# Kernel tuning notes

Hardware: AMD Instinct MI355X
Metric: run time of the kernel (lower is better)

The kernel has to match this reference:

```python
import jax, jax.numpy as jnp
import numpy as np

MULT = 32       # multiplicity per irrep type (both input and output)
N = 262144      # number of nodes/examples
LS = (0, 1, 2, 3)  # irrep degrees -> block sizes 2l+1 = 1,3,5,7


def setup_inputs() -> dict:
    key = jax.random.key(0)
    keys = jax.random.split(key, 2 * len(LS))
    inp = {}
    for j, l in enumerate(LS):
        m = 2 * l + 1
        inp[f"x{l}"] = jax.random.normal(keys[2 * j], (N, MULT, m), dtype=jnp.float32)
        inp[f"W{l}"] = jax.random.normal(keys[2 * j + 1], (MULT, MULT, m), dtype=jnp.float32)
    return inp


def reference(x0, x1, x2, x3, W0, W1, W2, W3):
    # Block-diagonal equivariant linear: for each irrep type l,
    # out[n, o, m] = sum_i W_l[o, i, m] * x_l[n, i, m]
    # (elementwise in m within each 2l+1 block, summed over input multiplicity i).
    outs = [
        jnp.einsum("nim,oim->nom", x, W)
        for x, W in ((x0, W0), (x1, W1), (x2, W2), (x3, W3))
    ]
    # Concatenate flattened irrep blocks -> [N, MULT*(1+3+5+7)] = [N, 512]
    return jnp.concatenate([o.reshape(o.shape[0], -1) for o in outs], axis=-1)
```

## Files before the change

### kernel.cpp

```cpp
#include <hip/hip_runtime.h>
#include <hip/hip_fp16.h>


#define NTH 512
#define TN  32

typedef _Float16 f16x8 __attribute__((ext_vector_type(8)));
typedef float    f32x4 __attribute__((ext_vector_type(4)));

template<int M_, int PB>
__device__ __forceinline__ void stage(const float* __restrict__ src,
                                      __half* __restrict__ dst, int tid)
{
    #pragma unroll
    for (int it = 0; it < (256 * M_ + NTH - 1) / NTH; ++it) {
        const int f = tid + it * NTH;
        if (f < 256 * M_) {
            float4 v = ((const float4*)src)[f];
            const int e0 = 4 * f;
            if (M_ == 1) {
                const int node = e0 >> 5, i = e0 & 31;
                __half2* p = (__half2*)(dst + node * 40 + i);
                p[0] = __floats2half2_rn(v.x, v.y);
                p[1] = __floats2half2_rn(v.z, v.w);
            } else {
                const float vf[4] = {v.x, v.y, v.z, v.w};
                #pragma unroll
                for (int k = 0; k < 4; ++k) {
                    const int e    = e0 + k;
                    const int node = e / (32 * M_);
                    const int r    = e - node * (32 * M_);
                    const int i    = r / M_, mi = r - i * M_;
                    dst[(PB + mi) * 1280 + node * 40 + i] = __float2half(vf[k]);
                }
            }
        }
    }
}

__device__ __forceinline__ void plane_info(int p, int& Mm, int& BASE, int& MI)
{
    if (p == 0)     { Mm = 1; BASE = 0;   MI = 0;     }
    else if (p < 4) { Mm = 3; BASE = 32;  MI = p - 1; }
    else if (p < 9) { Mm = 5; BASE = 128; MI = p - 4; }
    else            { Mm = 7; BASE = 288; MI = p - 9; }
}

__global__ __launch_bounds__(NTH, 4) void eqlin(
    const float* __restrict__ x0, const float* __restrict__ x1,
    const float* __restrict__ x2, const float* __restrict__ x3,
    const float* __restrict__ w0, const float* __restrict__ w1,
    const float* __restrict__ w2, const float* __restrict__ w3,
    float* __restrict__ out, int n_tiles)
{
    __shared__ __align__(16) __half XT[20480];
    __shared__ __align__(16) __half WT[20480];
    const int tid  = threadIdx.x;
    const int wave = tid >> 6;
    const int lane = tid & 63;

    stage<1, 0>(w0, WT, tid);
    stage<3, 1>(w1, WT, tid);
    stage<5, 4>(w2, WT, tid);
    stage<7, 9>(w3, WT, tid);

    int Mm0, BASE0, MI0, Mm1, BASE1, MI1;
    plane_info(wave * 2,     Mm0, BASE0, MI0);
    plane_info(wave * 2 + 1, Mm1, BASE1, MI1);

    const int lrow = lane & 15;
    const int lk8  = (lane >> 4) * 8;
    const int crow = (lane >> 4) * 4;

    for (int t = blockIdx.x; t < n_tiles; t += gridDim.x) {
        const long node0 = (long)t * TN;
        __syncthreads();
        stage<1, 0>(x0 + node0 * 32,  XT, tid);
        stage<3, 1>(x1 + node0 * 96,  XT, tid);
        stage<5, 4>(x2 + node0 * 160, XT, tid);
        stage<7, 9>(x3 + node0 * 224, XT, tid);
        __syncthreads();

        f32x4 acc[2][2][2] = {};
        #pragma unroll
        for (int pl = 0; pl < 2; ++pl) {
            const int plane = wave * 2 + pl;
            const __half* xb = XT + plane * 1280 + lrow * 40 + lk8;
            const __half* wb = WT + plane * 1280 + lrow * 40 + lk8;
            f16x8 A0 = *(const f16x8*)xb;
            f16x8 A1 = *(const f16x8*)(xb + 640);
            f16x8 B0 = *(const f16x8*)wb;
            f16x8 B1 = *(const f16x8*)(wb + 640);
            acc[pl][0][0] = __builtin_amdgcn_mfma_f32_16x16x32_f16(A0, B0, acc[pl][0][0], 0, 0, 0);
            acc[pl][0][1] = __builtin_amdgcn_mfma_f32_16x16x32_f16(A0, B1, acc[pl][0][1], 0, 0, 0);
            acc[pl][1][0] = __builtin_amdgcn_mfma_f32_16x16x32_f16(A1, B0, acc[pl][1][0], 0, 0, 0);
            acc[pl][1][1] = __builtin_amdgcn_mfma_f32_16x16x32_f16(A1, B1, acc[pl][1][1], 0, 0, 0);
        }
        __syncthreads();

        __half* OUT = XT;
        #pragma unroll
        for (int pl = 0; pl < 2; ++pl) {
            const int Mm   = pl ? Mm1   : Mm0;
            const int BASE = pl ? BASE1 : BASE0;
            const int MI   = pl ? MI1   : MI0;
            #pragma unroll
            for (int nh = 0; nh < 2; ++nh)
            #pragma unroll
            for (int oh = 0; oh < 2; ++oh) {
                const int o     = oh * 16 + lrow;
                const int colb  = BASE + o * Mm + MI;
                const int nodeb = nh * 16 + crow;
                #pragma unroll
                for (int r = 0; r < 4; ++r)
                    OUT[(nodeb + r) * 520 + colb] = __float2half(acc[pl][nh][oh][r]);
            }
        }
        __syncthreads();

        float* dst = out + node0 * 512;
        #pragma unroll
        for (int it = 0; it < 4; ++it) {
            const int d0   = 8 * tid + 4096 * it;
            const int node = d0 >> 9, col = d0 & 511;
            uint4 h8 = *(const uint4*)(OUT + node * 520 + col);
            const __half2* hp = (const __half2*)&h8;
            float2 f0 = __half22float2(hp[0]);
            float2 f1 = __half22float2(hp[1]);
            float2 f2 = __half22float2(hp[2]);
            float2 f3 = __half22float2(hp[3]);
            *(float4*)(dst + d0)     = make_float4(f0.x, f0.y, f1.x, f1.y);
            *(float4*)(dst + d0 + 4) = make_float4(f2.x, f2.y, f3.x, f3.y);
        }
    }
}

extern "C" void kernel_launch(void* const* d_in, const int* in_sizes, int n_in,
                              void* d_out, int out_size, void* d_ws, size_t ws_size,
                              hipStream_t stream)
{
    long tot = 0;
    for (int i = 0; i < n_in; ++i) tot += in_sizes[i];
    const long N = (tot - 16384) / 512;
    const int  ms[4] = {1, 3, 5, 7};
    const float* xs[4]  = {nullptr, nullptr, nullptr, nullptr};
    const float* wsp[4] = {nullptr, nullptr, nullptr, nullptr};
    for (int i = 0; i < n_in; ++i) {
        const long s = in_sizes[i];
        for (int l = 0; l < 4; ++l) {
            if (s == N * 32 * ms[l])      xs[l]  = (const float*)d_in[i];
            else if (s == 1024L * ms[l])  wsp[l] = (const float*)d_in[i];
        }
    }
    const int n_tiles = (int)(N / TN);
    const int grid = 512;
    hipLaunchKernelGGL(eqlin, dim3(grid), dim3(NTH), 0, stream,
                       xs[0], xs[1], xs[2], xs[3],
                       wsp[0], wsp[1], wsp[2], wsp[3],
                       (float*)d_out, n_tiles);
}
```

Measured before the change: 231.6 us.

## Prefetch next tile's inputs into registers and use LDS-only barriers

Each thread is assigned a fixed slice of one irrep input and precomputes its LDS scatter offsets once. The next tile's global loads are issued into registers before the current tile's compute and stores, overlapping HBM latency with work. __syncthreads is replaced by an lgkmcnt(0) wait plus s_barrier so barriers do not wait on outstanding global loads. The cost is more registers held across the loop (8 float4 per thread), which may reduce occupancy.

```diff
diff --git a/kernel.cpp b/kernel.cpp
--- a/kernel.cpp
+++ b/kernel.cpp
@@ -8,33 +8,42 @@
 typedef _Float16 f16x8 __attribute__((ext_vector_type(8)));
 typedef float    f32x4 __attribute__((ext_vector_type(4)));
 
+#define LGKM0_BAR() do { asm volatile("s_waitcnt lgkmcnt(0)" ::: "memory"); \
+                         __builtin_amdgcn_s_barrier(); } while (0)
+
 template<int M_, int PB>
-__device__ __forceinline__ void stage(const float* __restrict__ src,
-                                      __half* __restrict__ dst, int tid)
+__device__ __forceinline__ void stageW(const float* __restrict__ src,
+                                       __half* __restrict__ dst, int tid)
 {
     #pragma unroll
     for (int it = 0; it < (256 * M_ + NTH - 1) / NTH; ++it) {
         const int f = tid + it * NTH;
         if (f < 256 * M_) {
             float4 v = ((const float4*)src)[f];
+            const float vf[4] = {v.x, v.y, v.z, v.w};
             const int e0 = 4 * f;
-            if (M_ == 1) {
-                const int node = e0 >> 5, i = e0 & 31;
-                __half2* p = (__half2*)(dst + node * 40 + i);
-                p[0] = __floats2half2_rn(v.x, v.y);
-                p[1] = __floats2half2_rn(v.z, v.w);
-            } else {
-                const float vf[4] = {v.x, v.y, v.z, v.w};
-                #pragma unroll
-                for (int k = 0; k < 4; ++k) {
-                    const int e    = e0 + k;
-                    const int node = e / (32 * M_);
-                    const int r    = e - node * (32 * M_);
-                    const int i    = r / M_, mi = r - i * M_;
-                    dst[(PB + mi) * 1280 + node * 40 + i] = __float2half(vf[k]);
-                }
+            #pragma unroll
+            for (int k = 0; k < 4; ++k) {
+                const int e = e0 + k;
+                const int o = e / (32 * M_);
+                const int r = e - o * (32 * M_);
+                const int i = r / M_, mi = r - i * M_;
+                dst[(PB + mi) * 1280 + o * 40 + i] = __float2half(vf[k]);
             }
         }
+    }
+}
+
+template<int M_, int PB>
+__device__ __forceinline__ void mkoff(int tloc, int* offk)
+{
+    const int e0    = 4 * tloc;
+    const int nodel = e0 / (32 * M_);
+    const int r0    = e0 - nodel * (32 * M_);
+    #pragma unroll
+    for (int k = 0; k < 4; ++k) {
+        const int ii = (r0 + k) / M_, mi = (r0 + k) - ii * M_;
+        offk[k] = (PB + mi) * 1280 + nodel * 40 + ii;
     }
 }
 
@@ -59,44 +68,82 @@
     const int wave = tid >> 6;
     const int lane = tid & 63;
 
-    stage<1, 0>(w0, WT, tid);
-    stage<3, 1>(w1, WT, tid);
-    stage<5, 4>(w2, WT, tid);
-    stage<7, 9>(w3, WT, tid);
+    int thrg, Mg, offk[4];
+    const float* xb;
+    bool isM1 = false;
+    if (tid < 32)       { thrg = 32;  Mg = 1; xb = x0; mkoff<1, 0>(tid,       offk); isM1 = true; }
+    else if (tid < 128) { thrg = 96;  Mg = 3; xb = x1; mkoff<3, 1>(tid - 32,  offk); }
+    else if (tid < 288) { thrg = 160; Mg = 5; xb = x2; mkoff<5, 4>(tid - 128, offk); }
+    else                { thrg = 224; Mg = 7; xb = x3; mkoff<7, 9>(tid - 288, offk); }
+    const int  tloc    = (tid < 32) ? tid : (tid < 128) ? tid - 32 : (tid < 288) ? tid - 128 : tid - 288;
+    const long jstride = 4L * thrg;
+    const long tstride = (long)gridDim.x * 1024L * Mg;
+
+    const float* srcp = xb + (long)blockIdx.x * (1024L * Mg) + 4 * tloc;
+    float4 pf[8];
+    #pragma unroll
+    for (int j = 0; j < 8; ++j)
+        pf[j] = *(const float4*)(srcp + j * jstride);
+
+    stageW<1, 0>(w0, WT, tid);
+    stageW<3, 1>(w1, WT, tid);
+    stageW<5, 4>(w2, WT, tid);
+    stageW<7, 9>(w3, WT, tid);
 
     int Mm0, BASE0, MI0, Mm1, BASE1, MI1;
     plane_info(wave * 2,     Mm0, BASE0, MI0);
     plane_info(wave * 2 + 1, Mm1, BASE1, MI1);
-
     const int lrow = lane & 15;
     const int lk8  = (lane >> 4) * 8;
     const int crow = (lane >> 4) * 4;
 
     for (int t = blockIdx.x; t < n_tiles; t += gridDim.x) {
         const long node0 = (long)t * TN;
-        __syncthreads();
-        stage<1, 0>(x0 + node0 * 32,  XT, tid);
-        stage<3, 1>(x1 + node0 * 96,  XT, tid);
-        stage<5, 4>(x2 + node0 * 160, XT, tid);
-        stage<7, 9>(x3 + node0 * 224, XT, tid);
-        __syncthreads();
+
+        LGKM0_BAR();
+
+        #pragma unroll
+        for (int j = 0; j < 8; ++j) {
+            const float4 v = pf[j];
+            const int jb = j * 160;
+            if (isM1) {
+                __half2* p = (__half2*)&XT[offk[0] + jb];
+                p[0] = __floats2half2_rn(v.x, v.y);
+                p[1] = __floats2half2_rn(v.z, v.w);
+            } else {
+                XT[offk[0] + jb] = __float2half(v.x);
+                XT[offk[1] + jb] = __float2half(v.y);
+                XT[offk[2] + jb] = __float2half(v.z);
+                XT[offk[3] + jb] = __float2half(v.w);
+            }
+        }
+
+        if (t + (long)gridDim.x < n_tiles) {
+            srcp += tstride;
+            #pragma unroll
+            for (int j = 0; j < 8; ++j)
+                pf[j] = *(const float4*)(srcp + j * jstride);
+        }
+
+        LGKM0_BAR();
 
         f32x4 acc[2][2][2] = {};
         #pragma unroll
         for (int pl = 0; pl < 2; ++pl) {
             const int plane = wave * 2 + pl;
-            const __half* xb = XT + plane * 1280 + lrow * 40 + lk8;
-            const __half* wb = WT + plane * 1280 + lrow * 40 + lk8;
-            f16x8 A0 = *(const f16x8*)xb;
-            f16x8 A1 = *(const f16x8*)(xb + 640);
-            f16x8 B0 = *(const f16x8*)wb;
-            f16x8 B1 = *(const f16x8*)(wb + 640);
+            const __half* xp = XT + plane * 1280 + lrow * 40 + lk8;
+            const __half* wp = WT + plane * 1280 + lrow * 40 + lk8;
+            f16x8 A0 = *(const f16x8*)xp;
+            f16x8 A1 = *(const f16x8*)(xp + 640);
+            f16x8 B0 = *(const f16x8*)wp;
+            f16x8 B1 = *(const f16x8*)(wp + 640);
             acc[pl][0][0] = __builtin_amdgcn_mfma_f32_16x16x32_f16(A0, B0, acc[pl][0][0], 0, 0, 0);
             acc[pl][0][1] = __builtin_amdgcn_mfma_f32_16x16x32_f16(A0, B1, acc[pl][0][1], 0, 0, 0);
             acc[pl][1][0] = __builtin_amdgcn_mfma_f32_16x16x32_f16(A1, B0, acc[pl][1][0], 0, 0, 0);
             acc[pl][1][1] = __builtin_amdgcn_mfma_f32_16x16x32_f16(A1, B1, acc[pl][1][1], 0, 0, 0);
         }
-        __syncthreads();
+
+        LGKM0_BAR();
 
         __half* OUT = XT;
         #pragma unroll
@@ -116,7 +163,8 @@
                     OUT[(nodeb + r) * 520 + colb] = __float2half(acc[pl][nh][oh][r]);
             }
         }
-        __syncthreads();
+
+        LGKM0_BAR();
 
         float* dst = out + node0 * 512;
         #pragma unroll
```

New measurement: 217.0 us. 1.07x faster.
